# Kernel optimization log

Hardware: AMD Instinct MI355X
Metric: run time of the kernel (lower is better)

Reference implementation:

```python
import jax, jax.numpy as jnp
import numpy as np
from jax import lax

NEG = -1000.0  # torch.full((N,S), -1000.0) init in dp_align


def setup_inputs() -> dict:
    key = jax.random.key(0)
    ks = jax.random.split(key, 4)
    N, S, h = 128, 2048, 256          # nodes, segments, hsize
    d = 2 * h                         # bi-LSTM output dim = 2*hsize
    seg_text_feats = jax.random.normal(ks[0], (N, d), jnp.float32)
    vid_feature = jax.random.normal(ks[1], (S, d), jnp.float32)
    # relation_query: Linear(4h, h) -> ReLU -> (Dropout, eval=identity) -> Linear(h, 1)
    W1 = jax.random.normal(ks[2], (h, 2 * d), jnp.float32) / np.sqrt(2.0 * d)
    b1 = jnp.zeros((h,), jnp.float32)
    W2 = jax.random.normal(ks[3], (1, h), jnp.float32) / np.sqrt(float(h))
    b2 = jnp.zeros((1,), jnp.float32)
    return {"seg_text_feats": seg_text_feats, "vid_feature": vid_feature,
            "W1": W1, "b1": b1, "W2": W2, "b2": b2}


def reference(seg_text_feats, vid_feature, W1, b1, W2, b2):
    N, d = seg_text_feats.shape
    S = vid_feature.shape[0]
    # Pairwise MLP logits for every (node, segment) cell, vectorized:
    # concat(text, vid) @ W1^T == text @ W1[:, :d]^T + vid @ W1[:, d:]^T
    A = seg_text_feats @ W1[:, :d].T           # [N, h]
    B = vid_feature @ W1[:, d:].T              # [S, h]
    H = jax.nn.relu(A[:, None, :] + B[None, :, :] + b1)   # [N, S, h]
    logits = jnp.einsum('nsh,h->ns', H, W2[0]) + b2[0]     # [N, S]
    logsig = jax.nn.log_sigmoid(logits)

    n_idx = jnp.arange(N)
    # DP over columns, right to left. prev_col is arr[:, s+1] (virtual col S = NEG).
    def step(prev_col, s):
        ls = logsig[:, s]
        nxt = jnp.concatenate([prev_col[1:], jnp.full((1,), NEG, prev_col.dtype)])  # arr[n+1, s+1]
        curr = ls + jnp.where(n_idx == N - 1, 0.0, nxt)   # last node: no chain term
        take = curr >= prev_col                            # tie -> take current (matches >=)
        val = jnp.where(take, curr, prev_col)
        in_range = (s >= n_idx) & (s <= S - N + n_idx)     # start_ind/end_ind bands
        col = jnp.where(in_range, val, NEG)
        return col, take

    _, takes = lax.scan(step, jnp.full((N,), NEG), jnp.arange(S - 1, -1, -1))
    take_curr = takes[::-1].T                              # [N, S]

    # Backtrack parent pointers from (node 0, segment 0).
    def walk(carry, s):
        n, align = carry
        nc = jnp.minimum(n, N - 1)
        tc = take_curr[nc, s] & (n < N)
        align = align.at[nc].set(jnp.where(tc, s, align[nc]))
        return (n + tc.astype(jnp.int32), align), None

    (_, align), _ = lax.scan(walk, (jnp.int32(0), jnp.zeros((N,), jnp.int32)), jnp.arange(S))

    aggregated_logits = jnp.mean(logits[n_idx, align])     # sum(logit)/num_nodes
    adj_matrix = jnp.zeros((N + S, N + S), jnp.float32).at[S + n_idx, align].set(1.0)
    return adj_matrix, aggregated_logits
```

## Files before the change

kernel.cpp:

```cpp
#include <hip/hip_runtime.h>
#include <math.h>

#define NEGC (-1000.0f)
#define MAGICA 0x5137A9C1u
#define MAGICB 0x2468ACE1u
#define MAGICC 0x13579BDFu

__global__ __launch_bounds__(512, 1) void kA(
    const float* __restrict__ seg, const float* __restrict__ vid,
    const float* __restrict__ W1, const float* __restrict__ b1,
    const float* __restrict__ W2, const float* __restrict__ b2p,
    float* __restrict__ A2, float* __restrict__ B2,
    float* __restrict__ logitsT, float* __restrict__ lsPK,
    unsigned* __restrict__ flags)
{
    __shared__ float Xs[32][64];
    __shared__ float Ws[32][64];
    __shared__ float w2s[256];
    const int bid = blockIdx.x;
    const int tid = threadIdx.x;
    const int tx = tid & 15;
    const int ty = tid >> 4;
    const int lr8 = tid >> 3;
    const int lk8 = (tid & 7) * 4;

    {
        const int colBase = (bid & 3) * 64;
        const int rowBase = (bid >> 2) * 64;
        const bool isSeg = (rowBase < 128);
        const float* __restrict__ X = isSeg ? seg : vid;
        const int xRow = isSeg ? rowBase : (rowBase - 128);
        const int wOff = isSeg ? 0 : 512;

        float acc[2][4] = {};
        float4 xa = *(const float4*)(X + (size_t)(xRow + lr8) * 512 + lk8);
        float4 wa = *(const float4*)(W1 + (size_t)(colBase + lr8) * 1024 + (wOff + lk8));

        for (int k0 = 0; k0 < 512; k0 += 32) {
            __syncthreads();
            Xs[lk8 + 0][lr8] = xa.x; Xs[lk8 + 1][lr8] = xa.y;
            Xs[lk8 + 2][lr8] = xa.z; Xs[lk8 + 3][lr8] = xa.w;
            Ws[lk8 + 0][lr8] = wa.x; Ws[lk8 + 1][lr8] = wa.y;
            Ws[lk8 + 2][lr8] = wa.z; Ws[lk8 + 3][lr8] = wa.w;
            __syncthreads();
            if (k0 + 32 < 512) {
                xa = *(const float4*)(X + (size_t)(xRow + lr8) * 512 + (k0 + 32 + lk8));
                wa = *(const float4*)(W1 + (size_t)(colBase + lr8) * 1024 + (wOff + k0 + 32 + lk8));
            }
            #pragma unroll
            for (int kk = 0; kk < 32; ++kk) {
                const float2 a2 = *(const float2*)&Xs[kk][2 * ty];
                const float4 b4 = *(const float4*)&Ws[kk][4 * tx];
                const float* a = (const float*)&a2;
                const float* b = (const float*)&b4;
                #pragma unroll
                for (int i = 0; i < 2; ++i)
                    #pragma unroll
                    for (int j = 0; j < 4; ++j)
                        acc[i][j] = fmaf(a[i], b[j], acc[i][j]);
            }
        }

        float* __restrict__ outp = (isSeg ? A2 : B2) + (size_t)xRow * 256;
        const int c = colBase + 4 * tx;
        #pragma unroll
        for (int i = 0; i < 2; ++i) {
            float4 v = make_float4(acc[i][0], acc[i][1], acc[i][2], acc[i][3]);
            if (isSeg) {
                v.x += b1[c + 0]; v.y += b1[c + 1]; v.z += b1[c + 2]; v.w += b1[c + 3];
            }
            *(float4*)(outp + (size_t)(2 * ty + i) * 256 + c) = v;
        }
    }

    __syncthreads();
    if (tid == 0)
        __hip_atomic_store(&flags[bid], MAGICA, __ATOMIC_RELEASE, __HIP_MEMORY_SCOPE_AGENT);
    if (bid == 0) {
        if (tid < 136) {
            while (__hip_atomic_load(&flags[tid], __ATOMIC_ACQUIRE,
                                     __HIP_MEMORY_SCOPE_AGENT) != MAGICA)
                __builtin_amdgcn_s_sleep(2);
        }
        __syncthreads();
        if (tid == 0)
            __hip_atomic_store(&flags[200], MAGICB, __ATOMIC_RELEASE, __HIP_MEMORY_SCOPE_AGENT);
    }
    if (bid >= 128) return;
    if (tid == 0) {
        while (__hip_atomic_load(&flags[200], __ATOMIC_ACQUIRE,
                                 __HIP_MEMORY_SCOPE_AGENT) != MAGICB)
            __builtin_amdgcn_s_sleep(2);
    }
    __syncthreads();

    {
        const int nBase = (bid & 1) * 64;
        const int sBase = (bid >> 1) * 32;
        if (tid < 256) w2s[tid] = W2[tid];
        const float b2v = b2p[0];

        float acc[2][2] = {};
        float4 aa = *(const float4*)(A2 + (size_t)(nBase + lr8) * 256 + lk8);
        float4 ba;
        if (tid < 256) ba = *(const float4*)(B2 + (size_t)(sBase + lr8) * 256 + lk8);

        for (int k0 = 0; k0 < 256; k0 += 32) {
            __syncthreads();
            Xs[lk8 + 0][lr8] = aa.x; Xs[lk8 + 1][lr8] = aa.y;
            Xs[lk8 + 2][lr8] = aa.z; Xs[lk8 + 3][lr8] = aa.w;
            if (tid < 256) {
                Ws[lk8 + 0][lr8] = ba.x; Ws[lk8 + 1][lr8] = ba.y;
                Ws[lk8 + 2][lr8] = ba.z; Ws[lk8 + 3][lr8] = ba.w;
            }
            __syncthreads();
            if (k0 + 32 < 256) {
                aa = *(const float4*)(A2 + (size_t)(nBase + lr8) * 256 + (k0 + 32 + lk8));
                if (tid < 256)
                    ba = *(const float4*)(B2 + (size_t)(sBase + lr8) * 256 + (k0 + 32 + lk8));
            }
            #pragma unroll
            for (int kk = 0; kk < 32; ++kk) {
                const float w = w2s[k0 + kk];
                const float2 a2 = *(const float2*)&Xs[kk][2 * ty];
                const float2 b2 = *(const float2*)&Ws[kk][2 * tx];
                const float* a = (const float*)&a2;
                const float* b = (const float*)&b2;
                #pragma unroll
                for (int i = 0; i < 2; ++i)
                    #pragma unroll
                    for (int j = 0; j < 2; ++j)
                        acc[i][j] = fmaf(fmaxf(a[i] + b[j], 0.0f), w, acc[i][j]);
            }
        }

        const int nb = nBase + 2 * ty;
        const int s0 = sBase + 2 * tx;
        float lsv[2][2];
        #pragma unroll
        for (int j = 0; j < 2; ++j) {
            float2 lg;
            float* lgp = (float*)&lg;
            #pragma unroll
            for (int i = 0; i < 2; ++i) {
                const float x = acc[i][j] + b2v;
                lgp[i] = x;
                lsv[j][i] = fminf(x, 0.0f) - log1pf(expf(-fabsf(x)));
            }
            *(float2*)&logitsT[(size_t)(s0 + j) * 128 + nb] = lg;
        }
        float4 pk = make_float4(lsv[0][0], lsv[1][0], lsv[0][1], lsv[1][1]);
        *(float4*)&lsPK[(size_t)(s0 / 2) * 256 + 2 * nb] = pk;
    }
}

__global__ __launch_bounds__(256, 1) void k3_dp(
    const float* __restrict__ lsPK, const float* __restrict__ logitsT,
    float* __restrict__ out, unsigned* __restrict__ flags2)
{
    __shared__ unsigned takeW[128 * 65];
    const int bid = blockIdx.x;
    const int tid = threadIdx.x;

    if (bid != 0) {
        float4* out4 = (float4*)out;
        const float4 z = make_float4(0.f, 0.f, 0.f, 0.f);
        const int start = (bid - 1) * 4642;
        const int count = (bid == 255) ? 4676 : 4642;
        for (int i = tid; i < count; i += 256) out4[start + i] = z;
        __syncthreads();
        if (tid == 0)
            __hip_atomic_store(&flags2[bid], MAGICC, __ATOMIC_RELEASE, __HIP_MEMORY_SCOPE_AGENT);
        return;
    }
    if (tid >= 64) return;

    const int lane = tid;
    const int n0 = 2 * lane, n1 = n0 + 1;
    const float4* __restrict__ ls4 = (const float4*)lsPK;

    float p0 = NEGC, p1 = NEGC;
    unsigned u0 = 2047u - (unsigned)n0;
    unsigned u1 = u0 - 1u;
    unsigned w0 = 0u, w1 = 0u;

    auto core = [&](float lx, float ly, float nx) {
        float c0, c1;
        unsigned long long cc;
        asm volatile(
            "v_add_f32 %[c0], %[lx], %[p1]\n\t"
            "v_add_f32 %[c1], %[ly], %[nx]\n\t"
            "v_cmp_ge_f32 vcc, %[c0], %[p0]\n\t"
            "v_cmp_ge_f32 %[cc], %[c1], %[p1]\n\t"
            "v_addc_co_u32 %[w0], vcc, %[w0], %[w0], vcc\n\t"
            "v_addc_co_u32 %[w1], %[cc], %[w1], %[w1], %[cc]\n\t"
            "v_max_f32 %[p0], %[c0], %[p0]\n\t"
            "v_max_f32 %[p1], %[c1], %[p1]\n\t"
            : [p0]"+v"(p0), [p1]"+v"(p1), [w0]"+v"(w0), [w1]"+v"(w1),
              [c0]"=&v"(c0), [c1]"=&v"(c1), [cc]"=&s"(cc)
            : [lx]"v"(lx), [ly]"v"(ly), [nx]"v"(nx)
            : "vcc");
    };

    auto stepF = [&](float lx, float ly) {
        float nxt1 = __int_as_float(__builtin_amdgcn_update_dpp(
            0, __float_as_int(p0), 0x130 , 0xf, 0xf, true));
        core(lx, ly, nxt1);
    };
    auto stepM = [&](float lx, float ly) {
        float nxt1 = __int_as_float(__builtin_amdgcn_update_dpp(
            0, __float_as_int(p0), 0x130, 0xf, 0xf, true));
        core(lx, ly, nxt1);
        p0 = (u0 <= 1920u) ? p0 : NEGC;
        p1 = (u1 <= 1920u) ? p1 : NEGC;
        --u0; --u1;
    };

    float4 B0[4], B1[4], B2r[4], B3[4], B4[4], B5[4], B6[4], B7[4];
    int wIdx = 63;
#define LOADG(B, H) { _Pragma("unroll") \
    for (int j = 0; j < 4; ++j) B[j] = ls4[(size_t)((1023 - 4 * (H) - j) * 64 + lane)]; }
#define STEPS_F(B) { _Pragma("unroll") \
    for (int j = 0; j < 4; ++j) { stepF(B[j].y, B[j].w); stepF(B[j].x, B[j].z); } }
#define STEPS_M(B) { _Pragma("unroll") \
    for (int j = 0; j < 4; ++j) { stepM(B[j].y, B[j].w); stepM(B[j].x, B[j].z); } }
#define FLUSH { takeW[n0 * 65 + wIdx] = w0; takeW[n1 * 65 + wIdx] = w1; \
                w0 = 0u; w1 = 0u; --wIdx; }
#define BODY(SM) \
    SM(B0);  if (h +  8 < 256) LOADG(B0,  h +  8); \
    SM(B1);  if (h +  9 < 256) LOADG(B1,  h +  9); \
    SM(B2r); if (h + 10 < 256) LOADG(B2r, h + 10); \
    SM(B3);  FLUSH; if (h + 11 < 256) LOADG(B3, h + 11); \
    SM(B4);  if (h + 12 < 256) LOADG(B4,  h + 12); \
    SM(B5);  if (h + 13 < 256) LOADG(B5,  h + 13); \
    SM(B6);  if (h + 14 < 256) LOADG(B6,  h + 14); \
    SM(B7);  FLUSH; if (h + 15 < 256) LOADG(B7, h + 15);

    LOADG(B0, 0) LOADG(B1, 1) LOADG(B2r, 2) LOADG(B3, 3)
    LOADG(B4, 4) LOADG(B5, 5) LOADG(B6, 6) LOADG(B7, 7)
    for (int h = 0; h < 16; h += 8) { BODY(STEPS_M) }
    for (int h = 16; h < 240; h += 8) { BODY(STEPS_F) }
    u0 = (unsigned)(127 - n0);
    u1 = u0 - 1u;
    for (int h = 240; h < 256; h += 8) { BODY(STEPS_M) }
#undef BODY
#undef FLUSH
#undef STEPS_M
#undef STEPS_F
#undef LOADG

    int a0r = 0, a1r = 0, pos = 0;
    for (int n = 0; n < 128; ++n) {
        unsigned w = takeW[n * 65 + lane];
        const int wi0 = pos >> 5;
        if (lane < wi0) w = 0u;
        else if (lane == wi0) w &= (0xFFFFFFFFu << (pos & 31));
        const unsigned long long m = __ballot(w != 0u);
        if (m == 0ull) break;
        const int fl = __builtin_ctzll(m);
        const unsigned fw = (unsigned)__builtin_amdgcn_readlane((int)w, fl);
        const int s = fl * 32 + __builtin_ctz(fw);
        if (n == n0) a0r = s;
        if (n == n1) a1r = s;
        pos = s + 1;
    }

    #pragma unroll
    for (int r = 0; r < 4; ++r) {
        const int idx = 1 + r * 64 + lane;
        if (idx <= 255) {
            while (__hip_atomic_load(&flags2[idx], __ATOMIC_ACQUIRE,
                                     __HIP_MEMORY_SCOPE_AGENT) != MAGICC)
                __builtin_amdgcn_s_sleep(2);
        }
    }

    out[(size_t)(2048 + n0) * 2176 + a0r] = 1.0f;
    out[(size_t)(2048 + n1) * 2176 + a1r] = 1.0f;
    float sum = logitsT[(size_t)a0r * 128 + n0] + logitsT[(size_t)a1r * 128 + n1];
    #pragma unroll
    for (int off = 32; off >= 1; off >>= 1) sum += __shfl_down(sum, off);
    if (lane == 0) out[(size_t)2176 * 2176] = sum * (1.0f / 128.0f);
}

extern "C" void kernel_launch(void* const* d_in, const int* in_sizes, int n_in,
                              void* d_out, int out_size, void* d_ws, size_t ws_size,
                              hipStream_t stream)
{
    const float* seg = (const float*)d_in[0];
    const float* vid = (const float*)d_in[1];
    const float* W1  = (const float*)d_in[2];
    const float* b1  = (const float*)d_in[3];
    const float* W2  = (const float*)d_in[4];
    const float* b2  = (const float*)d_in[5];
    float* out = (float*)d_out;
    float* ws  = (float*)d_ws;

    float* A2      = ws;
    float* B2      = ws + 32768;
    float* logitsT = ws + 557056;
    float* lsPK    = ws + 819200;
    unsigned* flags  = (unsigned*)(ws + 1081344);
    unsigned* flags2 = (unsigned*)(ws + 1081600);

    kA<<<dim3(136), dim3(512), 0, stream>>>(seg, vid, W1, b1, W2, b2,
                                            A2, B2, logitsT, lsPK, flags);
    k3_dp<<<dim3(256), dim3(256), 0, stream>>>(lsPK, logitsT, out, flags2);
}
```

Measured before the change: 199.3 us.

## Fuse GEMM and DP kernels into one launch with per-window readiness flags

Merges the two kernels into a single 256-block launch. Blocks 0-135 compute the projections and logits, and blocks 136-255 zero the output matrix. The DP block starts once its first column window of log-sigmoid values is published and then waits on per-block flags for each later window. This removes a kernel launch boundary and lets the serial DP overlap with logit production and output zeroing. The cost is more spin-waiting, and the design relies on all blocks being co-resident.

```diff
diff --git a/kernel.cpp b/kernel.cpp
--- a/kernel.cpp
+++ b/kernel.cpp
@@ -5,219 +5,228 @@
 #define MAGICA 0x5137A9C1u
 #define MAGICB 0x2468ACE1u
 #define MAGICC 0x13579BDFu
-
-__global__ __launch_bounds__(512, 1) void kA(
+#define MAGICD 0x0F1E2D3Cu
+
+__global__ __launch_bounds__(512, 1) void kall(
     const float* __restrict__ seg, const float* __restrict__ vid,
     const float* __restrict__ W1, const float* __restrict__ b1,
     const float* __restrict__ W2, const float* __restrict__ b2p,
     float* __restrict__ A2, float* __restrict__ B2,
     float* __restrict__ logitsT, float* __restrict__ lsPK,
-    unsigned* __restrict__ flags)
+    float* __restrict__ out, unsigned* __restrict__ flags)
 {
-    __shared__ float Xs[32][64];
-    __shared__ float Ws[32][64];
-    __shared__ float w2s[256];
+    __shared__ __align__(16) char smem[33280];
     const int bid = blockIdx.x;
     const int tid = threadIdx.x;
-    const int tx = tid & 15;
-    const int ty = tid >> 4;
-    const int lr8 = tid >> 3;
-    const int lk8 = (tid & 7) * 4;
-
-    {
-        const int colBase = (bid & 3) * 64;
-        const int rowBase = (bid >> 2) * 64;
-        const bool isSeg = (rowBase < 128);
-        const float* __restrict__ X = isSeg ? seg : vid;
-        const int xRow = isSeg ? rowBase : (rowBase - 128);
-        const int wOff = isSeg ? 0 : 512;
-
-        float acc[2][4] = {};
-        float4 xa = *(const float4*)(X + (size_t)(xRow + lr8) * 512 + lk8);
-        float4 wa = *(const float4*)(W1 + (size_t)(colBase + lr8) * 1024 + (wOff + lk8));
-
-        for (int k0 = 0; k0 < 512; k0 += 32) {
-            __syncthreads();
-            Xs[lk8 + 0][lr8] = xa.x; Xs[lk8 + 1][lr8] = xa.y;
-            Xs[lk8 + 2][lr8] = xa.z; Xs[lk8 + 3][lr8] = xa.w;
-            Ws[lk8 + 0][lr8] = wa.x; Ws[lk8 + 1][lr8] = wa.y;
-            Ws[lk8 + 2][lr8] = wa.z; Ws[lk8 + 3][lr8] = wa.w;
-            __syncthreads();
-            if (k0 + 32 < 512) {
-                xa = *(const float4*)(X + (size_t)(xRow + lr8) * 512 + (k0 + 32 + lk8));
-                wa = *(const float4*)(W1 + (size_t)(colBase + lr8) * 1024 + (wOff + k0 + 32 + lk8));
-            }
+
+    if (bid < 136) {
+        auto Xs = (float (*)[64])smem;
+        auto Ws = (float (*)[64])(smem + 8192);
+        float* w2s = (float*)(smem + 16384);
+        const int tx = tid & 15;
+        const int ty = tid >> 4;
+        const int lr8 = tid >> 3;
+        const int lk8 = (tid & 7) * 4;
+
+        {
+            const int colBase = (bid & 3) * 64;
+            const int rowBase = (bid >> 2) * 64;
+            const bool isSeg = (rowBase < 128);
+            const float* __restrict__ X = isSeg ? seg : vid;
+            const int xRow = isSeg ? rowBase : (rowBase - 128);
+            const int wOff = isSeg ? 0 : 512;
+
+            float acc[2][4] = {};
+            float4 xa = *(const float4*)(X + (size_t)(xRow + lr8) * 512 + lk8);
+            float4 wa = *(const float4*)(W1 + (size_t)(colBase + lr8) * 1024 + (wOff + lk8));
+
+            for (int k0 = 0; k0 < 512; k0 += 32) {
+                __syncthreads();
+                Xs[lk8 + 0][lr8] = xa.x; Xs[lk8 + 1][lr8] = xa.y;
+                Xs[lk8 + 2][lr8] = xa.z; Xs[lk8 + 3][lr8] = xa.w;
+                Ws[lk8 + 0][lr8] = wa.x; Ws[lk8 + 1][lr8] = wa.y;
+                Ws[lk8 + 2][lr8] = wa.z; Ws[lk8 + 3][lr8] = wa.w;
+                __syncthreads();
+                if (k0 + 32 < 512) {
+                    xa = *(const float4*)(X + (size_t)(xRow + lr8) * 512 + (k0 + 32 + lk8));
+                    wa = *(const float4*)(W1 + (size_t)(colBase + lr8) * 1024 + (wOff + k0 + 32 + lk8));
+                }
+                #pragma unroll
+                for (int kk = 0; kk < 32; ++kk) {
+                    const float2 a2 = *(const float2*)&Xs[kk][2 * ty];
+                    const float4 b4 = *(const float4*)&Ws[kk][4 * tx];
+                    const float* a = (const float*)&a2;
+                    const float* b = (const float*)&b4;
+                    #pragma unroll
+                    for (int i = 0; i < 2; ++i)
+                        #pragma unroll
+                        for (int j = 0; j < 4; ++j)
+                            acc[i][j] = fmaf(a[i], b[j], acc[i][j]);
+                }
+            }
+
+            float* __restrict__ outp = (isSeg ? A2 : B2) + (size_t)xRow * 256;
+            const int c = colBase + 4 * tx;
             #pragma unroll
-            for (int kk = 0; kk < 32; ++kk) {
-                const float2 a2 = *(const float2*)&Xs[kk][2 * ty];
-                const float4 b4 = *(const float4*)&Ws[kk][4 * tx];
-                const float* a = (const float*)&a2;
-                const float* b = (const float*)&b4;
-                #pragma unroll
-                for (int i = 0; i < 2; ++i)
-                    #pragma unroll
-                    for (int j = 0; j < 4; ++j)
-                        acc[i][j] = fmaf(a[i], b[j], acc[i][j]);
-            }
-        }
-
-        float* __restrict__ outp = (isSeg ? A2 : B2) + (size_t)xRow * 256;
-        const int c = colBase + 4 * tx;
-        #pragma unroll
-        for (int i = 0; i < 2; ++i) {
-            float4 v = make_float4(acc[i][0], acc[i][1], acc[i][2], acc[i][3]);
-            if (isSeg) {
-                v.x += b1[c + 0]; v.y += b1[c + 1]; v.z += b1[c + 2]; v.w += b1[c + 3];
-            }
-            *(float4*)(outp + (size_t)(2 * ty + i) * 256 + c) = v;
-        }
-    }
-
-    __syncthreads();
-    if (tid == 0)
-        __hip_atomic_store(&flags[bid], MAGICA, __ATOMIC_RELEASE, __HIP_MEMORY_SCOPE_AGENT);
-    if (bid == 0) {
-        if (tid < 136) {
-            while (__hip_atomic_load(&flags[tid], __ATOMIC_ACQUIRE,
-                                     __HIP_MEMORY_SCOPE_AGENT) != MAGICA)
-                __builtin_amdgcn_s_sleep(2);
-        }
+            for (int i = 0; i < 2; ++i) {
+                float4 v = make_float4(acc[i][0], acc[i][1], acc[i][2], acc[i][3]);
+                if (isSeg) {
+                    v.x += b1[c + 0]; v.y += b1[c + 1]; v.z += b1[c + 2]; v.w += b1[c + 3];
+                }
+                *(float4*)(outp + (size_t)(2 * ty + i) * 256 + c) = v;
+            }
+        }
+
         __syncthreads();
         if (tid == 0)
-            __hip_atomic_store(&flags[200], MAGICB, __ATOMIC_RELEASE, __HIP_MEMORY_SCOPE_AGENT);
+            __hip_atomic_store(&flags[bid], MAGICA, __ATOMIC_RELEASE, __HIP_MEMORY_SCOPE_AGENT);
+        if (bid == 0) {
+            if (tid < 136) {
+                while (__hip_atomic_load(&flags[tid], __ATOMIC_ACQUIRE,
+                                         __HIP_MEMORY_SCOPE_AGENT) != MAGICA)
+                    __builtin_amdgcn_s_sleep(2);
+            }
+            __syncthreads();
+            if (tid == 0)
+                __hip_atomic_store(&flags[200], MAGICB, __ATOMIC_RELEASE, __HIP_MEMORY_SCOPE_AGENT);
+        }
+        if (bid >= 128) return;
+        if (tid == 0) {
+            while (__hip_atomic_load(&flags[200], __ATOMIC_ACQUIRE,
+                                     __HIP_MEMORY_SCOPE_AGENT) != MAGICB)
+                __builtin_amdgcn_s_sleep(2);
+        }
+        __syncthreads();
+
+        {
+            const int nBase = (bid & 1) * 64;
+            const int sBase = (bid >> 1) * 32;
+            if (tid < 256) w2s[tid] = W2[tid];
+            const float b2v = b2p[0];
+
+            float acc[2][2] = {};
+            float4 aa = *(const float4*)(A2 + (size_t)(nBase + lr8) * 256 + lk8);
+            float4 ba;
+            if (tid < 256) ba = *(const float4*)(B2 + (size_t)(sBase + lr8) * 256 + lk8);
+
+            for (int k0 = 0; k0 < 256; k0 += 32) {
+                __syncthreads();
+                Xs[lk8 + 0][lr8] = aa.x; Xs[lk8 + 1][lr8] = aa.y;
+                Xs[lk8 + 2][lr8] = aa.z; Xs[lk8 + 3][lr8] = aa.w;
+                if (tid < 256) {
+                    Ws[lk8 + 0][lr8] = ba.x; Ws[lk8 + 1][lr8] = ba.y;
+                    Ws[lk8 + 2][lr8] = ba.z; Ws[lk8 + 3][lr8] = ba.w;
+                }
+                __syncthreads();
+                if (k0 + 32 < 256) {
+                    aa = *(const float4*)(A2 + (size_t)(nBase + lr8) * 256 + (k0 + 32 + lk8));
+                    if (tid < 256)
+                        ba = *(const float4*)(B2 + (size_t)(sBase + lr8) * 256 + (k0 + 32 + lk8));
+                }
+                #pragma unroll
+                for (int kk = 0; kk < 32; ++kk) {
+                    const float w = w2s[k0 + kk];
+                    const float2 a2 = *(const float2*)&Xs[kk][2 * ty];
+                    const float2 b2 = *(const float2*)&Ws[kk][2 * tx];
+                    const float* a = (const float*)&a2;
+                    const float* b = (const float*)&b2;
+                    #pragma unroll
+                    for (int i = 0; i < 2; ++i)
+                        #pragma unroll
+                        for (int j = 0; j < 2; ++j)
+                            acc[i][j] = fmaf(fmaxf(a[i] + b[j], 0.0f), w, acc[i][j]);
+                }
+            }
+
+            const int nb = nBase + 2 * ty;
+            const int s0 = sBase + 2 * tx;
+            float lsv[2][2];
+            #pragma unroll
+            for (int j = 0; j < 2; ++j) {
+                float2 lg;
+                float* lgp = (float*)&lg;
+                #pragma unroll
+                for (int i = 0; i < 2; ++i) {
+                    const float x = acc[i][j] + b2v;
+                    lgp[i] = x;
+                    lsv[j][i] = fminf(x, 0.0f) - log1pf(expf(-fabsf(x)));
+                }
+                *(float2*)&logitsT[(size_t)(s0 + j) * 128 + nb] = lg;
+            }
+            float4 pk = make_float4(lsv[0][0], lsv[1][0], lsv[0][1], lsv[1][1]);
+            *(float4*)&lsPK[(size_t)(s0 / 2) * 256 + 2 * nb] = pk;
+        }
+        __syncthreads();
+        if (tid == 0)
+            __hip_atomic_store(&flags[256 + bid], MAGICD, __ATOMIC_RELEASE, __HIP_MEMORY_SCOPE_AGENT);
+        return;
     }
-    if (bid >= 128) return;
-    if (tid == 0) {
-        while (__hip_atomic_load(&flags[200], __ATOMIC_ACQUIRE,
-                                 __HIP_MEMORY_SCOPE_AGENT) != MAGICB)
-            __builtin_amdgcn_s_sleep(2);
-    }
-    __syncthreads();
 
     {
-        const int nBase = (bid & 1) * 64;
-        const int sBase = (bid >> 1) * 32;
-        if (tid < 256) w2s[tid] = W2[tid];
-        const float b2v = b2p[0];
-
-        float acc[2][2] = {};
-        float4 aa = *(const float4*)(A2 + (size_t)(nBase + lr8) * 256 + lk8);
-        float4 ba;
-        if (tid < 256) ba = *(const float4*)(B2 + (size_t)(sBase + lr8) * 256 + lk8);
-
-        for (int k0 = 0; k0 < 256; k0 += 32) {
-            __syncthreads();
-            Xs[lk8 + 0][lr8] = aa.x; Xs[lk8 + 1][lr8] = aa.y;
-            Xs[lk8 + 2][lr8] = aa.z; Xs[lk8 + 3][lr8] = aa.w;
-            if (tid < 256) {
-                Ws[lk8 + 0][lr8] = ba.x; Ws[lk8 + 1][lr8] = ba.y;
-                Ws[lk8 + 2][lr8] = ba.z; Ws[lk8 + 3][lr8] = ba.w;
-            }
-            __syncthreads();
-            if (k0 + 32 < 256) {
-                aa = *(const float4*)(A2 + (size_t)(nBase + lr8) * 256 + (k0 + 32 + lk8));
-                if (tid < 256)
-                    ba = *(const float4*)(B2 + (size_t)(sBase + lr8) * 256 + (k0 + 32 + lk8));
-            }
-            #pragma unroll
-            for (int kk = 0; kk < 32; ++kk) {
-                const float w = w2s[k0 + kk];
-                const float2 a2 = *(const float2*)&Xs[kk][2 * ty];
-                const float2 b2 = *(const float2*)&Ws[kk][2 * tx];
-                const float* a = (const float*)&a2;
-                const float* b = (const float*)&b2;
-                #pragma unroll
-                for (int i = 0; i < 2; ++i)
-                    #pragma unroll
-                    for (int j = 0; j < 2; ++j)
-                        acc[i][j] = fmaf(fmaxf(a[i] + b[j], 0.0f), w, acc[i][j]);
-            }
-        }
-
-        const int nb = nBase + 2 * ty;
-        const int s0 = sBase + 2 * tx;
-        float lsv[2][2];
-        #pragma unroll
-        for (int j = 0; j < 2; ++j) {
-            float2 lg;
-            float* lgp = (float*)&lg;
-            #pragma unroll
-            for (int i = 0; i < 2; ++i) {
-                const float x = acc[i][j] + b2v;
-                lgp[i] = x;
-                lsv[j][i] = fminf(x, 0.0f) - log1pf(expf(-fabsf(x)));
-            }
-            *(float2*)&logitsT[(size_t)(s0 + j) * 128 + nb] = lg;
-        }
-        float4 pk = make_float4(lsv[0][0], lsv[1][0], lsv[0][1], lsv[1][1]);
-        *(float4*)&lsPK[(size_t)(s0 / 2) * 256 + 2 * nb] = pk;
-    }
-}
-
-__global__ __launch_bounds__(256, 1) void k3_dp(
-    const float* __restrict__ lsPK, const float* __restrict__ logitsT,
-    float* __restrict__ out, unsigned* __restrict__ flags2)
-{
-    __shared__ unsigned takeW[128 * 65];
-    const int bid = blockIdx.x;
-    const int tid = threadIdx.x;
-
-    if (bid != 0) {
         float4* out4 = (float4*)out;
         const float4 z = make_float4(0.f, 0.f, 0.f, 0.f);
-        const int start = (bid - 1) * 4642;
-        const int count = (bid == 255) ? 4676 : 4642;
-        for (int i = tid; i < count; i += 256) out4[start + i] = z;
+        const int start = (bid - 136) * 9865;
+        const int end = (start + 9865 < 1183744) ? start + 9865 : 1183744;
+        for (int i = start + tid; i < end; i += 512) out4[i] = z;
         __syncthreads();
         if (tid == 0)
-            __hip_atomic_store(&flags2[bid], MAGICC, __ATOMIC_RELEASE, __HIP_MEMORY_SCOPE_AGENT);
-        return;
+            __hip_atomic_store(&flags[384 + bid], MAGICC, __ATOMIC_RELEASE, __HIP_MEMORY_SCOPE_AGENT);
+        if (bid != 255) return;
     }
     if (tid >= 64) return;
 
-    const int lane = tid;
-    const int n0 = 2 * lane, n1 = n0 + 1;
-    const float4* __restrict__ ls4 = (const float4*)lsPK;
-
-    float p0 = NEGC, p1 = NEGC;
-    unsigned u0 = 2047u - (unsigned)n0;
-    unsigned u1 = u0 - 1u;
-    unsigned w0 = 0u, w1 = 0u;
-
-    auto core = [&](float lx, float ly, float nx) {
-        float c0, c1;
-        unsigned long long cc;
-        asm volatile(
-            "v_add_f32 %[c0], %[lx], %[p1]\n\t"
-            "v_add_f32 %[c1], %[ly], %[nx]\n\t"
-            "v_cmp_ge_f32 vcc, %[c0], %[p0]\n\t"
-            "v_cmp_ge_f32 %[cc], %[c1], %[p1]\n\t"
-            "v_addc_co_u32 %[w0], vcc, %[w0], %[w0], vcc\n\t"
-            "v_addc_co_u32 %[w1], %[cc], %[w1], %[w1], %[cc]\n\t"
-            "v_max_f32 %[p0], %[c0], %[p0]\n\t"
-            "v_max_f32 %[p1], %[c1], %[p1]\n\t"
-            : [p0]"+v"(p0), [p1]"+v"(p1), [w0]"+v"(w0), [w1]"+v"(w1),
-              [c0]"=&v"(c0), [c1]"=&v"(c1), [cc]"=&s"(cc)
-            : [lx]"v"(lx), [ly]"v"(ly), [nx]"v"(nx)
-            : "vcc");
-    };
-
-    auto stepF = [&](float lx, float ly) {
-        float nxt1 = __int_as_float(__builtin_amdgcn_update_dpp(
-            0, __float_as_int(p0), 0x130 , 0xf, 0xf, true));
-        core(lx, ly, nxt1);
-    };
-    auto stepM = [&](float lx, float ly) {
-        float nxt1 = __int_as_float(__builtin_amdgcn_update_dpp(
-            0, __float_as_int(p0), 0x130, 0xf, 0xf, true));
-        core(lx, ly, nxt1);
-        p0 = (u0 <= 1920u) ? p0 : NEGC;
-        p1 = (u1 <= 1920u) ? p1 : NEGC;
-        --u0; --u1;
-    };
-
-    float4 B0[4], B1[4], B2r[4], B3[4], B4[4], B5[4], B6[4], B7[4];
-    int wIdx = 63;
+    {
+        unsigned* takeW = (unsigned*)smem;
+        const int lane = tid;
+        const int n0 = 2 * lane, n1 = n0 + 1;
+        const float4* __restrict__ ls4 = (const float4*)lsPK;
+
+        float p0 = NEGC, p1 = NEGC;
+        unsigned u0 = 2047u - (unsigned)n0;
+        unsigned u1 = u0 - 1u;
+        unsigned w0 = 0u, w1 = 0u;
+
+        auto core = [&](float lx, float ly, float nx) {
+            float c0, c1;
+            unsigned long long cc;
+            asm volatile(
+                "v_add_f32 %[c0], %[lx], %[p1]\n\t"
+                "v_add_f32 %[c1], %[ly], %[nx]\n\t"
+                "v_cmp_ge_f32 vcc, %[c0], %[p0]\n\t"
+                "v_cmp_ge_f32 %[cc], %[c1], %[p1]\n\t"
+                "v_addc_co_u32 %[w0], vcc, %[w0], %[w0], vcc\n\t"
+                "v_addc_co_u32 %[w1], %[cc], %[w1], %[w1], %[cc]\n\t"
+                "v_max_f32 %[p0], %[c0], %[p0]\n\t"
+                "v_max_f32 %[p1], %[c1], %[p1]\n\t"
+                : [p0]"+v"(p0), [p1]"+v"(p1), [w0]"+v"(w0), [w1]"+v"(w1),
+                  [c0]"=&v"(c0), [c1]"=&v"(c1), [cc]"=&s"(cc)
+                : [lx]"v"(lx), [ly]"v"(ly), [nx]"v"(nx)
+                : "vcc");
+        };
+
+        auto stepF = [&](float lx, float ly) {
+            float nxt1 = __int_as_float(__builtin_amdgcn_update_dpp(
+                0, __float_as_int(p0), 0x130 , 0xf, 0xf, true));
+            core(lx, ly, nxt1);
+        };
+        auto stepM = [&](float lx, float ly) {
+            float nxt1 = __int_as_float(__builtin_amdgcn_update_dpp(
+                0, __float_as_int(p0), 0x130, 0xf, 0xf, true));
+            core(lx, ly, nxt1);
+            p0 = (u0 <= 1920u) ? p0 : NEGC;
+            p1 = (u1 <= 1920u) ? p1 : NEGC;
+            --u0; --u1;
+        };
+
+        auto waitWin = [&](int g) {
+            const unsigned* tf = &flags[256 + 120 - 8 * g];
+            while (__hip_atomic_load(&tf[lane & 7], __ATOMIC_ACQUIRE,
+                                     __HIP_MEMORY_SCOPE_AGENT) != MAGICD)
+                __builtin_amdgcn_s_sleep(2);
+        };
+
+        float4 B0[4], B1[4], B2r[4], B3[4], B4[4], B5[4], B6[4], B7[4];
+        int wIdx = 63;
 #define LOADG(B, H) { _Pragma("unroll") \
     for (int j = 0; j < 4; ++j) B[j] = ls4[(size_t)((1023 - 4 * (H) - j) * 64 + lane)]; }
 #define STEPS_F(B) { _Pragma("unroll") \
@@ -235,52 +244,56 @@
     SM(B5);  if (h + 13 < 256) LOADG(B5,  h + 13); \
     SM(B6);  if (h + 14 < 256) LOADG(B6,  h + 14); \
     SM(B7);  FLUSH; if (h + 15 < 256) LOADG(B7, h + 15);
-
-    LOADG(B0, 0) LOADG(B1, 1) LOADG(B2r, 2) LOADG(B3, 3)
-    LOADG(B4, 4) LOADG(B5, 5) LOADG(B6, 6) LOADG(B7, 7)
-    for (int h = 0; h < 16; h += 8) { BODY(STEPS_M) }
-    for (int h = 16; h < 240; h += 8) { BODY(STEPS_F) }
-    u0 = (unsigned)(127 - n0);
-    u1 = u0 - 1u;
-    for (int h = 240; h < 256; h += 8) { BODY(STEPS_M) }
+#define GATE { int gw = (h + 15) >> 4; if (gw > 15) gw = 15; waitWin(gw); }
+
+        waitWin(0);
+        LOADG(B0, 0) LOADG(B1, 1) LOADG(B2r, 2) LOADG(B3, 3)
+        LOADG(B4, 4) LOADG(B5, 5) LOADG(B6, 6) LOADG(B7, 7)
+        for (int h = 0; h < 16; h += 8) { GATE BODY(STEPS_M) }
+        for (int h = 16; h < 240; h += 8) { GATE BODY(STEPS_F) }
+        u0 = (unsigned)(127 - n0);
+        u1 = u0 - 1u;
+        for (int h = 240; h < 256; h += 8) { GATE BODY(STEPS_M) }
+#undef GATE
 #undef BODY
 #undef FLUSH
 #undef STEPS_M
 #undef STEPS_F
 #undef LOADG
 
-    int a0r = 0, a1r = 0, pos = 0;
-    for (int n = 0; n < 128; ++n) {
-        unsigned w = takeW[n * 65 + lane];
-        const int wi0 = pos >> 5;
-        if (lane < wi0) w = 0u;
-        else if (lane == wi0) w &= (0xFFFFFFFFu << (pos & 31));
-        const unsigned long long m = __ballot(w != 0u);
-        if (m == 0ull) break;
-        const int fl = __builtin_ctzll(m);
-        const unsigned fw = (unsigned)__builtin_amdgcn_readlane((int)w, fl);
-        const int s = fl * 32 + __builtin_ctz(fw);
-        if (n == n0) a0r = s;
-        if (n == n1) a1r = s;
-        pos = s + 1;
+        int a0r = 0, a1r = 0, pos = 0;
+        for (int n = 0; n < 128; ++n) {
+            unsigned w = takeW[n * 65 + lane];
+            const int wi0 = pos >> 5;
+            if (lane < wi0) w = 0u;
+            else if (lane == wi0) w &= (0xFFFFFFFFu << (pos & 31));
+            const unsigned long long m = __ballot(w != 0u);
+            if (m == 0ull) break;
+            const int fl = __builtin_ctzll(m);
+            const unsigned fw = (unsigned)__builtin_amdgcn_readlane((int)w, fl);
+            const int s = fl * 32 + __builtin_ctz(fw);
+            if (n == n0) a0r = s;
+            if (n == n1) a1r = s;
+            pos = s + 1;
+        }
+
+        #pragma unroll
+        for (int r = 0; r < 2; ++r) {
+            const int idx = 136 + r * 64 + lane;
+            if (idx <= 255) {
+                while (__hip_atomic_load(&flags[384 + idx], __ATOMIC_ACQUIRE,
+                                         __HIP_MEMORY_SCOPE_AGENT) != MAGICC)
+                    __builtin_amdgcn_s_sleep(2);
+            }
+        }
+
+        out[(size_t)(2048 + n0) * 2176 + a0r] = 1.0f;
+        out[(size_t)(2048 + n1) * 2176 + a1r] = 1.0f;
+        float sum = logitsT[(size_t)a0r * 128 + n0] + logitsT[(size_t)a1r * 128 + n1];
+        #pragma unroll
+        for (int off = 32; off >= 1; off >>= 1) sum += __shfl_down(sum, off);
+        if (lane == 0) out[(size_t)2176 * 2176] = sum * (1.0f / 128.0f);
     }
-
-    #pragma unroll
-    for (int r = 0; r < 4; ++r) {
-        const int idx = 1 + r * 64 + lane;
-        if (idx <= 255) {
-            while (__hip_atomic_load(&flags2[idx], __ATOMIC_ACQUIRE,
-                                     __HIP_MEMORY_SCOPE_AGENT) != MAGICC)
-                __builtin_amdgcn_s_sleep(2);
-        }
-    }
-
-    out[(size_t)(2048 + n0) * 2176 + a0r] = 1.0f;
-    out[(size_t)(2048 + n1) * 2176 + a1r] = 1.0f;
-    float sum = logitsT[(size_t)a0r * 128 + n0] + logitsT[(size_t)a1r * 128 + n1];
-    #pragma unroll
-    for (int off = 32; off >= 1; off >>= 1) sum += __shfl_down(sum, off);
-    if (lane == 0) out[(size_t)2176 * 2176] = sum * (1.0f / 128.0f);
 }
 
 extern "C" void kernel_launch(void* const* d_in, const int* in_sizes, int n_in,
@@ -300,10 +313,8 @@
     float* B2      = ws + 32768;
     float* logitsT = ws + 557056;
     float* lsPK    = ws + 819200;
-    unsigned* flags  = (unsigned*)(ws + 1081344);
-    unsigned* flags2 = (unsigned*)(ws + 1081600);
-
-    kA<<<dim3(136), dim3(512), 0, stream>>>(seg, vid, W1, b1, W2, b2,
-                                            A2, B2, logitsT, lsPK, flags);
-    k3_dp<<<dim3(256), dim3(256), 0, stream>>>(lsPK, logitsT, out, flags2);
+    unsigned* flags = (unsigned*)(ws + 1081344);
+
+    kall<<<dim3(256), dim3(512), 0, stream>>>(seg, vid, W1, b1, W2, b2,
+                                              A2, B2, logitsT, lsPK, out, flags);
 }
```

Measured after the change: 205.9 us. +3.3%, slower.
